# Kernel optimization log

Hardware: AMD Instinct MI355X
Metric: run time of the kernel (lower is better)

Reference implementation:

```python
import jax, jax.numpy as jnp
import numpy as np

WZ, WH, WW = 2, 6, 12
N = WZ * WH * WW            # 144 tokens per window
DIM, HEADS = 384, 12
HD = DIM // HEADS           # 32
TOW = (8 // WZ) * (48 // WH)  # type_of_windows = 32
NW = 96 // WW               # longitude windows = 8
B_ = 1 * TOW * NW           # 256
TABLE = (2 * WW - 1) * WH * WH * WZ * WZ  # 3312


def _position_index():
    zi = np.arange(WZ); zj = -np.arange(WZ) * WZ
    hi = np.arange(WH); hj = -np.arange(WH) * WH
    w = np.arange(WW)
    c1 = np.stack(np.meshgrid(zi, hi, w, indexing='ij')).reshape(3, -1)
    c2 = np.stack(np.meshgrid(zj, hj, w, indexing='ij')).reshape(3, -1)
    coords = (c1[:, :, None] - c2[:, None, :]).transpose(1, 2, 0)  # (N, N, 3)
    coords[:, :, 2] += WW - 1
    coords[:, :, 1] *= 2 * WW - 1
    coords[:, :, 0] *= (2 * WW - 1) * WH * WH
    return coords.sum(-1).reshape(-1).astype(np.int32)  # (N*N,)


def setup_inputs() -> dict:
    key = jax.random.key(0)
    ks = jax.random.split(key, 7)
    x = jax.random.normal(ks[0], (B_, N, DIM), dtype=jnp.float32)
    mask = jax.random.normal(ks[1], (NW, N, N), dtype=jnp.float32)
    w_qkv = jax.random.normal(ks[2], (DIM, 3 * DIM), dtype=jnp.float32) * 0.02
    b_qkv = jax.random.normal(ks[3], (3 * DIM,), dtype=jnp.float32) * 0.02
    w_out = jax.random.normal(ks[4], (DIM, DIM), dtype=jnp.float32) * 0.02
    b_out = jax.random.normal(ks[5], (DIM,), dtype=jnp.float32) * 0.02
    bias_table = jax.random.normal(ks[6], (TABLE, TOW, HEADS), dtype=jnp.float32) * 0.02
    position_index = jnp.asarray(_position_index())
    return {"x": x, "mask": mask, "w_qkv": w_qkv, "b_qkv": b_qkv,
            "w_out": w_out, "b_out": b_out, "bias_table": bias_table,
            "position_index": position_index}


def reference(x, mask, w_qkv, b_qkv, w_out, b_out, bias_table, position_index):
    Bw, n, C = x.shape
    scale = HD ** -0.5
    qkv = (x @ w_qkv + b_qkv).reshape(Bw, n, 3, HEADS, HD)
    qkv = jnp.transpose(qkv, (2, 0, 3, 1, 4))  # (3, Bw, H, N, hd)
    q, k, v = qkv[0] * scale, qkv[1], qkv[2]
    attn = jnp.einsum('bhnd,bhmd->bhnm', q, k)  # (Bw, H, N, N)
    # Earth-specific bias: gather table rows by position index, tiled per window group
    r = Bw // TOW
    bias = bias_table[jnp.tile(position_index, r)]          # (r*N*N, TOW, H)
    bias = bias.reshape(n, n, -1, HEADS)                    # (N, N, Bw, H)
    bias = jnp.transpose(bias, (2, 3, 0, 1))                # (Bw, H, N, N)
    attn = attn + bias
    nW = mask.shape[0]
    attn = attn.reshape(Bw // nW, nW, HEADS, n, n) + mask[None, :, None]
    attn = jax.nn.softmax(attn.reshape(Bw, HEADS, n, n), axis=-1)
    out = jnp.einsum('bhnm,bhmd->bhnd', attn, v)            # (Bw, H, N, hd)
    out = jnp.transpose(out, (0, 2, 1, 3)).reshape(Bw, n, C)
    return out @ w_out + b_out
```

## Files before the change

kernel.cpp:

```cpp
#include <hip/hip_runtime.h>
#include <hip/hip_fp16.h>
#include <cstdint>
#include <cstddef>

#define NQQ  (144*144)
#define SCALE 0.17677669529663687f

#define AOH   0ull
#define X16H  0ull
#define QH    14155776ull
#define KH    28311552ull
#define VH    42467328ull
#define WTH   56623104ull
#define WOTH  57065472ull
#define MASKH 57212928ull
#define BIASH 57378816ull
#define WS_NEED_BYTES ((BIASH + 3072ull * 2592ull) * 2ull)

typedef _Float16 half8  __attribute__((ext_vector_type(8)));
typedef _Float16 half4v __attribute__((ext_vector_type(4)));
typedef float    f32x4  __attribute__((ext_vector_type(4)));

typedef __attribute__((address_space(1))) const unsigned int guint;
typedef __attribute__((address_space(3))) unsigned int luint;
#define GLD16(g, l) __builtin_amdgcn_global_load_lds((guint*)(g), (luint*)(l), 16, 0, 0)

__launch_bounds__(256)
__global__ void k_prep(const float* __restrict__ X, _Float16* __restrict__ X16,
                       const float* __restrict__ Wq, _Float16* __restrict__ WqT,
                       const float* __restrict__ Wo, _Float16* __restrict__ WoT,
                       const float* __restrict__ M, _Float16* __restrict__ M16,
                       const float* __restrict__ table, const int* __restrict__ pidx,
                       _Float16* __restrict__ biasOut) {
    __shared__ __align__(16) char psm[13888];
    const int bid = blockIdx.x;
    const int t   = threadIdx.x;
    if (bid < 13824) {
        size_t i = (size_t)bid * 256 + t;
        float4 f = *(const float4*)&X[i * 4];
        _Float16 h[4] = {(_Float16)f.x, (_Float16)f.y, (_Float16)f.z, (_Float16)f.w};
        *(ushort4*)&X16[i * 4] = *(ushort4*)h;
        return;
    }
    if (bid >= 14130) {
        _Float16 (*sTb)[18] = (_Float16(*)[18])psm;
        int* rowsL = (int*)(psm + 13824);
        const int j      = bid - 14130;
        const int s_tile = j / 162;
        const int chunk  = j - s_tile * 162;
        const int i0     = chunk * 16;
        if (t < 16) rowsL[t] = pidx[8 * (i0 + t) + s_tile];
        __syncthreads();
#pragma unroll
        for (int rr = 0; rr < 16; ++rr) {
            int row = rowsL[rr];
            sTb[t][rr] = (_Float16)table[(size_t)row * 384 + t];
            if (t < 128) sTb[t + 256][rr] = (_Float16)table[(size_t)row * 384 + t + 256];
        }
        __syncthreads();
        unsigned int* ob = (unsigned int*)biasOut;
#pragma unroll
        for (int v = t; v < 3072; v += 256) {
            int i1h = v >> 3, dw = v & 7;
            ob[(size_t)(s_tile * 384 + i1h) * 1296 + chunk * 8 + dw] =
                *(const unsigned int*)&sTb[i1h][dw * 2];
        }
        return;
    }
    if (bid >= 13968) {
        size_t i = (size_t)(bid - 13968) * 256 + t;
        float4 f = *(const float4*)&M[i * 4];
        _Float16 h[4] = {(_Float16)f.x, (_Float16)f.y, (_Float16)f.z, (_Float16)f.w};
        *(ushort4*)&M16[i * 4] = *(ushort4*)h;
        return;
    }
    _Float16 (*sT)[72] = (_Float16(*)[72])psm;
    const float* W; _Float16* WT; int K, Cn, cb, kb;
    if (bid < 13932) {
        int j = bid - 13824;
        W = Wq; WT = WqT; K = 384; Cn = 1152;
        cb = (j % 18) * 64; kb = (j / 18) * 64;
    } else {
        int j = bid - 13932;
        W = Wo; WT = WoT; K = 384; Cn = 384;
        cb = (j % 6) * 64; kb = (j / 6) * 64;
    }
#pragma unroll
    for (int i = 0; i < 16; ++i) {
        int id = t + 256 * i;
        int kl = id >> 6, cl = id & 63;
        sT[cl][kl] = (_Float16)W[(size_t)(kb + kl) * Cn + cb + cl];
    }
    __syncthreads();
#pragma unroll
    for (int i = 0; i < 16; ++i) {
        int id = t + 256 * i;
        int cl = id >> 6, kl = id & 63;
        WT[(size_t)(cb + cl) * K + kb + kl] = sT[cl][kl];
    }
}

#define STAGE2(dA, dB, kk) do {                                   \
    GLD16(gA + (kk),          (char*)(dA) + t * 16);              \
    GLD16(gA + (kk) + 24576,  (char*)(dA) + t * 16 + 4096);       \
    GLD16(gB + (kk),          (char*)(dB) + t * 16);              \
    GLD16(gB + (kk) + 24576,  (char*)(dB) + t * 16 + 4096);       \
} while (0)

#define CSTEP(pA, pB) do {                                        \
    half8 a[4], b[4];                                             \
    _Pragma("unroll")                                             \
    for (int i = 0; i < 4; ++i) a[i] = *(const half8*)((pA) + i * 1024); \
    _Pragma("unroll")                                             \
    for (int j = 0; j < 4; ++j) b[j] = *(const half8*)((pB) + j * 1024); \
    _Pragma("unroll")                                             \
    for (int i = 0; i < 4; ++i)                                   \
    _Pragma("unroll")                                             \
        for (int j = 0; j < 4; ++j)                               \
            acc[i][j] = __builtin_amdgcn_mfma_f32_16x16x32_f16(a[i], b[j], acc[i][j], 0, 0, 0); \
} while (0)

__launch_bounds__(256)
__global__ void k_qkv_gemm_mfma(const _Float16* __restrict__ X16,
                                const _Float16* __restrict__ WT,
                                const float* __restrict__ bq,
                                _Float16* __restrict__ ws16) {
    __shared__ __align__(16) _Float16 sA0[4096], sB0[4096], sA1[4096], sB1[4096];
    const int t    = threadIdx.x;
    const int lane = t & 63;
    const int w    = t >> 6;
    const int quad = lane >> 4;
    const int l15  = lane & 15;
    const int bid = blockIdx.x;
    const int wg  = (bid & 7) * 324 + (bid >> 3);
    const int cy  = wg % 9, rx = wg / 9;
    const int r0  = rx * 128, c0 = cy * 128;
    const int wr  = (w >> 1) * 64, wc = (w & 1) * 64;

    const int srow = t >> 2;
    const int skch = (t & 3) ^ ((t >> 3) & 3);
    const _Float16* gA = &X16[(size_t)(r0 + srow) * 384 + skch * 8];
    const _Float16* gB = &WT [(size_t)(c0 + srow) * 384 + skch * 8];

    const int swz16 = (quad ^ ((l15 >> 1) & 3)) * 16;
    const char* rA0 = (const char*)sA0 + (wr + l15) * 64 + swz16;
    const char* rA1 = (const char*)sA1 + (wr + l15) * 64 + swz16;
    const char* rB0 = (const char*)sB0 + (wc + l15) * 64 + swz16;
    const char* rB1 = (const char*)sB1 + (wc + l15) * 64 + swz16;

    f32x4 acc[4][4] = {};

    STAGE2(sA0, sB0, 0);
    __syncthreads();
#pragma unroll
    for (int s2 = 0; s2 < 6; ++s2) {
        STAGE2(sA1, sB1, 64 * s2 + 32);
        CSTEP(rA0, rB0);
        __syncthreads();
        if (s2 < 5) STAGE2(sA0, sB0, 64 * s2 + 64);
        CSTEP(rA1, rB1);
        __syncthreads();
    }

#pragma unroll
    for (int j = 0; j < 4; ++j) {
        int c  = c0 + wc + 16 * j + l15;
        int p  = c / 384;
        int hh = (c >> 5) % 12;
        int d0 = c & 31;
        float bias = bq[c];
        float sc   = (p == 0) ? SCALE : 1.0f;
        size_t base = (p == 0) ? QH : ((p == 1) ? KH : VH);
#pragma unroll
        for (int i = 0; i < 4; ++i) {
#pragma unroll
            for (int reg = 0; reg < 4; ++reg) {
                int r  = r0 + wr + 16 * i + quad * 4 + reg;
                int bw = r / 144;
                int n  = r - bw * 144;
                ws16[base + (((size_t)bw * 12 + hh) * 144 + n) * 32 + d0] =
                    (_Float16)((acc[i][j][reg] + bias) * sc);
            }
        }
    }
}

__launch_bounds__(576)
__global__ void k_attn_fused_mfma(const _Float16* __restrict__ ws16,
                                  const _Float16* __restrict__ mask16,
                                  const float* __restrict__ table,
                                  const int* __restrict__ pidx,
                                  const _Float16* __restrict__ bias_pre,
                                  _Float16* __restrict__ AO) {
    __shared__ __align__(16) char smem[27616];
    _Float16 (*sK)[40]   = (_Float16(*)[40])(smem);
    _Float16 (*sVT)[168] = (_Float16(*)[168])(smem + 11520);
    _Float16* sBias      = (_Float16*)(smem + 22272);

    const int bh = blockIdx.x;
    const int b  = bh / 12;
    const int h  = bh - b * 12;
    const int t  = threadIdx.x;
    const int w    = t >> 6;
    const int lane = t & 63;
    const int quad = lane >> 4;
    const int l15  = lane & 15;

    const int s_tile = b >> 5;
    const int i1     = b & 31;

    const _Float16* qg = ws16 + QH + (size_t)bh * 4608;
    const _Float16* kg = ws16 + KH + (size_t)bh * 4608;
    const _Float16* vg = ws16 + VH + (size_t)bh * 4608;

    half8 aq = *(const half8*)&qg[(size_t)(16 * w + l15) * 32 + quad * 8];

    {
        int row = t >> 2, ko = (t & 3) * 8;
        *(uint4*)&sK[row][ko] = *(const uint4*)&kg[row * 32 + ko];
    }
    for (int i = t; i < 2304; i += 576) {
        unsigned int u = ((const unsigned int*)vg)[i];
        int m  = i >> 4, d0 = (i & 15) * 2;
        int mp = m ^ ((d0 >> 3) << 3);
        sVT[d0][mp]     = ((const _Float16*)&u)[0];
        sVT[d0 + 1][mp] = ((const _Float16*)&u)[1];
    }
    if (t < 512) {
        int d = t & 31, m = 144 + (t >> 5);
        sVT[d][m ^ ((d >> 3) << 3)] = (_Float16)0;
    }
    if (bias_pre) {
        const _Float16* bg = bias_pre + (size_t)bh * 2592;
        for (int i2 = t; i2 < 648; i2 += 576) {
            uint2 wv = *(const uint2*)&bg[i2 * 4];
            int r18 = i2 / 36;
            int col = i2 * 4 - r18 * 144;
            *(uint2*)&sBias[r18 * 148 + col] = wv;
        }
    } else {
        for (int i = t; i < 2592; i += 576) {
            int row = pidx[8 * i + s_tile];
            int r18 = i / 144;
            sBias[r18 * 148 + (i - r18 * 144)] =
                (_Float16)table[(size_t)row * 384 + i1 * 12 + h];
        }
    }
    __syncthreads();

    f32x4 tj[9] = {};
#pragma unroll
    for (int j = 0; j < 9; ++j) {
        half8 bk = *(const half8*)&sK[16 * j + l15][quad * 8];
        tj[j] = __builtin_amdgcn_mfma_f32_16x16x32_f16(bk, aq, tj[j], 0, 0, 0);
    }

    const int q    = 16 * w + l15;
    const int nb18 = q % 18;
    const _Float16* mrow = mask16 + (size_t)(b & 7) * NQQ + (size_t)q * 144 + 4 * quad;
    uint2 mz[9];
#pragma unroll
    for (int j = 0; j < 9; ++j) mz[j] = *(const uint2*)&mrow[16 * j];
#pragma unroll
    for (int j = 0; j < 9; ++j) {
        uint2 bz = *(const uint2*)&sBias[nb18 * 148 + 16 * j + 4 * quad];
        const _Float16* bb = (const _Float16*)&bz;
        const _Float16* mm = (const _Float16*)&mz[j];
#pragma unroll
        for (int reg = 0; reg < 4; ++reg)
            tj[j][reg] += (float)bb[reg] + (float)mm[reg];
    }
    float rmax = tj[0][0];
#pragma unroll
    for (int j = 0; j < 9; ++j)
#pragma unroll
        for (int reg = 0; reg < 4; ++reg) rmax = fmaxf(rmax, tj[j][reg]);
    rmax = fmaxf(rmax, __shfl_xor(rmax, 16));
    rmax = fmaxf(rmax, __shfl_xor(rmax, 32));
    float rsum = 0.0f;
#pragma unroll
    for (int j = 0; j < 9; ++j)
#pragma unroll
        for (int reg = 0; reg < 4; ++reg) {
            tj[j][reg] = __expf(tj[j][reg] - rmax);
            rsum += tj[j][reg];
        }
    rsum += __shfl_xor(rsum, 16);
    rsum += __shfl_xor(rsum, 32);
    const float inv = 1.0f / rsum;

    unsigned int pkA[10], pkB[10];
    pkA[9] = 0u; pkB[9] = 0u;
#pragma unroll
    for (int j = 0; j < 9; ++j) {
        auto a2 = __builtin_amdgcn_cvt_pkrtz(tj[j][0] * inv, tj[j][1] * inv);
        auto b2 = __builtin_amdgcn_cvt_pkrtz(tj[j][2] * inv, tj[j][3] * inv);
        pkA[j] = *(unsigned int*)&a2;
        pkB[j] = *(unsigned int*)&b2;
    }

    const int src_lo = 32 * (quad & 1) + l15;
    const int src_hi = src_lo + 16;
    const bool selhi = (quad >> 1) != 0;
    f32x4 o[2] = {};
#pragma unroll
    for (int kt = 0; kt < 5; ++kt) {
        const int j0 = 2 * kt, j1 = 2 * kt + 1;
        unsigned int a0l = __shfl((int)pkA[j0], src_lo);
        unsigned int a1l = __shfl((int)pkA[j1], src_lo);
        unsigned int b0l = __shfl((int)pkB[j0], src_lo);
        unsigned int b1l = __shfl((int)pkB[j1], src_lo);
        unsigned int a0h = __shfl((int)pkA[j0], src_hi);
        unsigned int a1h = __shfl((int)pkA[j1], src_hi);
        unsigned int b0h = __shfl((int)pkB[j0], src_hi);
        unsigned int b1h = __shfl((int)pkB[j1], src_hi);
        union { uint4 u4; half8 h8; } bp;
        bp.u4.x = selhi ? a1l : a0l;
        bp.u4.y = selhi ? b1l : b0l;
        bp.u4.z = selhi ? a1h : a0h;
        bp.u4.w = selhi ? b1h : b0h;
#pragma unroll
        for (int dt = 0; dt < 2; ++dt) {
            const int vrow = dt * 16 + l15;
            half8 av = *(const half8*)&sVT[vrow][(kt * 32 + quad * 8) ^ ((vrow >> 3) << 3)];
            o[dt] = __builtin_amdgcn_mfma_f32_16x16x32_f16(av, bp.h8, o[dt], 0, 0, 0);
        }
    }

#pragma unroll
    for (int dt = 0; dt < 2; ++dt) {
        int d = dt * 16 + quad * 4;
        half4v hv;
#pragma unroll
        for (int reg = 0; reg < 4; ++reg) hv[reg] = (_Float16)o[dt][reg];
        *(half4v*)&AO[((size_t)b * 144 + q) * 384 + h * 32 + d] = hv;
    }
}

__launch_bounds__(256)
__global__ void k_out_gemm_mfma(const _Float16* __restrict__ A16,
                                const _Float16* __restrict__ WoT,
                                const float* __restrict__ bo,
                                float* __restrict__ out) {
    __shared__ __align__(16) _Float16 sA0[4096], sB0[4096], sA1[4096], sB1[4096];
    const int t    = threadIdx.x;
    const int lane = t & 63;
    const int w    = t >> 6;
    const int quad = lane >> 4;
    const int l15  = lane & 15;
    const int bid = blockIdx.x;
    const int wg  = (bid & 7) * 108 + (bid >> 3);
    const int cy  = wg % 3, rx = wg / 3;
    const int r0  = rx * 128, c0 = cy * 128;
    const int wr  = (w >> 1) * 64, wc = (w & 1) * 64;

    const int srow = t >> 2;
    const int skch = (t & 3) ^ ((t >> 3) & 3);
    const _Float16* gA = &A16[(size_t)(r0 + srow) * 384 + skch * 8];
    const _Float16* gB = &WoT[(size_t)(c0 + srow) * 384 + skch * 8];

    const int swz16 = (quad ^ ((l15 >> 1) & 3)) * 16;
    const char* rA0 = (const char*)sA0 + (wr + l15) * 64 + swz16;
    const char* rA1 = (const char*)sA1 + (wr + l15) * 64 + swz16;
    const char* rB0 = (const char*)sB0 + (wc + l15) * 64 + swz16;
    const char* rB1 = (const char*)sB1 + (wc + l15) * 64 + swz16;

    f32x4 acc[4][4] = {};

    STAGE2(sA0, sB0, 0);
    __syncthreads();
#pragma unroll
    for (int s2 = 0; s2 < 6; ++s2) {
        STAGE2(sA1, sB1, 64 * s2 + 32);
        CSTEP(rA0, rB0);
        __syncthreads();
        if (s2 < 5) STAGE2(sA0, sB0, 64 * s2 + 64);
        CSTEP(rA1, rB1);
        __syncthreads();
    }

#pragma unroll
    for (int j = 0; j < 4; ++j) {
        int c = c0 + wc + 16 * j + l15;
        float bias = bo[c];
#pragma unroll
        for (int i = 0; i < 4; ++i) {
#pragma unroll
            for (int reg = 0; reg < 4; ++reg) {
                int r = r0 + wr + 16 * i + quad * 4 + reg;
                out[(size_t)r * 384 + c] = acc[i][j][reg] + bias;
            }
        }
    }
}

extern "C" void kernel_launch(void* const* d_in, const int* in_sizes, int n_in,
                              void* d_out, int out_size, void* d_ws, size_t ws_size,
                              hipStream_t stream) {
    const float* x      = (const float*)d_in[0];
    const float* mask   = (const float*)d_in[1];
    const float* w_qkv  = (const float*)d_in[2];
    const float* b_qkv  = (const float*)d_in[3];
    const float* w_out  = (const float*)d_in[4];
    const float* b_out  = (const float*)d_in[5];
    const float* table  = (const float*)d_in[6];
    const int*   pidx   = (const int*)d_in[7];
    float* out = (float*)d_out;
    _Float16* ws16 = (_Float16*)d_ws;

    const bool pre = ws_size >= (size_t)WS_NEED_BYTES;
    _Float16* bias16 = pre ? (ws16 + BIASH) : (_Float16*)nullptr;

    hipLaunchKernelGGL(k_prep,          dim3(pre ? 15426 : 14130), dim3(256), 0, stream,
                       x, ws16 + X16H, w_qkv, ws16 + WTH, w_out, ws16 + WOTH,
                       mask, ws16 + MASKH, table, pidx, bias16);
    hipLaunchKernelGGL(k_qkv_gemm_mfma, dim3(2592), dim3(256), 0, stream,
                       ws16 + X16H, ws16 + WTH, b_qkv, ws16);
    hipLaunchKernelGGL(k_attn_fused_mfma, dim3(3072), dim3(576), 0, stream,
                       ws16, ws16 + MASKH, table, pidx, bias16, ws16 + AOH);
    hipLaunchKernelGGL(k_out_gemm_mfma, dim3(864), dim3(256), 0, stream,
                       ws16 + AOH, ws16 + WOTH, b_out, out);
}
```

Baseline: 267.4 us.

## Triple-buffer GEMM LDS staging with partial vmcnt waits and single barrier

The QKV and output-projection MFMA GEMMs move from a double-buffered loop with two full __syncthreads per pair of k-steps to a three-stage ring of LDS buffers. Each step waits with s_waitcnt vmcnt(4), which leaves the next stage's async global-to-LDS loads in flight, then issues one s_barrier before computing. This aims to keep two tiles of loads outstanding so memory latency overlaps with MFMA work. The cost is 50% more LDS per block, which can lower occupancy, and the correctness now depends on hand-counted waitcnt values.

```diff
diff --git a/kernel.cpp b/kernel.cpp
--- a/kernel.cpp
+++ b/kernel.cpp
@@ -24,6 +24,9 @@
 typedef __attribute__((address_space(1))) const unsigned int guint;
 typedef __attribute__((address_space(3))) unsigned int luint;
 #define GLD16(g, l) __builtin_amdgcn_global_load_lds((guint*)(g), (luint*)(l), 16, 0, 0)
+
+#define WAITV4 asm volatile("s_waitcnt vmcnt(4)" ::: "memory")
+#define WAITV0 asm volatile("s_waitcnt vmcnt(0)" ::: "memory")
 
 __launch_bounds__(256)
 __global__ void k_prep(const float* __restrict__ X, _Float16* __restrict__ X16,
@@ -100,7 +103,7 @@
     }
 }
 
-#define STAGE2(dA, dB, kk) do {                                   \
+#define STAGE3(dA, dB, kk) do {                                   \
     GLD16(gA + (kk),          (char*)(dA) + t * 16);              \
     GLD16(gA + (kk) + 24576,  (char*)(dA) + t * 16 + 4096);       \
     GLD16(gB + (kk),          (char*)(dB) + t * 16);              \
@@ -120,12 +123,27 @@
             acc[i][j] = __builtin_amdgcn_mfma_f32_16x16x32_f16(a[i], b[j], acc[i][j], 0, 0, 0); \
 } while (0)
 
+#define GEMM_PIPE() do {                                          \
+    STAGE3(sA[0], sB[0], 0);                                      \
+    STAGE3(sA[1], sB[1], 32);                                     \
+    _Pragma("unroll")                                             \
+    for (int s = 0; s < 12; ++s) {                                \
+        if (s < 11) { WAITV4; } else { WAITV0; }                  \
+        __builtin_amdgcn_s_barrier();                             \
+        if (s < 10) STAGE3(sA[(s + 2) % 3], sB[(s + 2) % 3], 32 * (s + 2)); \
+        const char* pA = (const char*)sA[s % 3] + aoff;           \
+        const char* pB = (const char*)sB[s % 3] + boff;           \
+        CSTEP(pA, pB);                                            \
+    }                                                             \
+} while (0)
+
 __launch_bounds__(256)
 __global__ void k_qkv_gemm_mfma(const _Float16* __restrict__ X16,
                                 const _Float16* __restrict__ WT,
                                 const float* __restrict__ bq,
                                 _Float16* __restrict__ ws16) {
-    __shared__ __align__(16) _Float16 sA0[4096], sB0[4096], sA1[4096], sB1[4096];
+    __shared__ __align__(16) _Float16 sA[3][4096];
+    __shared__ __align__(16) _Float16 sB[3][4096];
     const int t    = threadIdx.x;
     const int lane = t & 63;
     const int w    = t >> 6;
@@ -143,24 +161,12 @@
     const _Float16* gB = &WT [(size_t)(c0 + srow) * 384 + skch * 8];
 
     const int swz16 = (quad ^ ((l15 >> 1) & 3)) * 16;
-    const char* rA0 = (const char*)sA0 + (wr + l15) * 64 + swz16;
-    const char* rA1 = (const char*)sA1 + (wr + l15) * 64 + swz16;
-    const char* rB0 = (const char*)sB0 + (wc + l15) * 64 + swz16;
-    const char* rB1 = (const char*)sB1 + (wc + l15) * 64 + swz16;
+    const int aoff  = (wr + l15) * 64 + swz16;
+    const int boff  = (wc + l15) * 64 + swz16;
 
     f32x4 acc[4][4] = {};
 
-    STAGE2(sA0, sB0, 0);
-    __syncthreads();
-#pragma unroll
-    for (int s2 = 0; s2 < 6; ++s2) {
-        STAGE2(sA1, sB1, 64 * s2 + 32);
-        CSTEP(rA0, rB0);
-        __syncthreads();
-        if (s2 < 5) STAGE2(sA0, sB0, 64 * s2 + 64);
-        CSTEP(rA1, rB1);
-        __syncthreads();
-    }
+    GEMM_PIPE();
 
 #pragma unroll
     for (int j = 0; j < 4; ++j) {
@@ -342,7 +348,8 @@
                                 const _Float16* __restrict__ WoT,
                                 const float* __restrict__ bo,
                                 float* __restrict__ out) {
-    __shared__ __align__(16) _Float16 sA0[4096], sB0[4096], sA1[4096], sB1[4096];
+    __shared__ __align__(16) _Float16 sA[3][4096];
+    __shared__ __align__(16) _Float16 sB[3][4096];
     const int t    = threadIdx.x;
     const int lane = t & 63;
     const int w    = t >> 6;
@@ -360,24 +367,12 @@
     const _Float16* gB = &WoT[(size_t)(c0 + srow) * 384 + skch * 8];
 
     const int swz16 = (quad ^ ((l15 >> 1) & 3)) * 16;
-    const char* rA0 = (const char*)sA0 + (wr + l15) * 64 + swz16;
-    const char* rA1 = (const char*)sA1 + (wr + l15) * 64 + swz16;
-    const char* rB0 = (const char*)sB0 + (wc + l15) * 64 + swz16;
-    const char* rB1 = (const char*)sB1 + (wc + l15) * 64 + swz16;
+    const int aoff  = (wr + l15) * 64 + swz16;
+    const int boff  = (wc + l15) * 64 + swz16;
 
     f32x4 acc[4][4] = {};
 
-    STAGE2(sA0, sB0, 0);
-    __syncthreads();
-#pragma unroll
-    for (int s2 = 0; s2 < 6; ++s2) {
-        STAGE2(sA1, sB1, 64 * s2 + 32);
-        CSTEP(rA0, rB0);
-        __syncthreads();
-        if (s2 < 5) STAGE2(sA0, sB0, 64 * s2 + 64);
-        CSTEP(rA1, rB1);
-        __syncthreads();
-    }
+    GEMM_PIPE();
 
 #pragma unroll
     for (int j = 0; j < 4; ++j) {
```

After: 259.4 us. 3.0% less time.
